# Kernel tuning notes

Hardware: AMD Instinct MI355X
Metric: run time of the kernel (lower is better)

The kernel has to match this reference:

```python
import jax, jax.numpy as jnp
import numpy as np

BLOCK = 32      # config.BLOCK_SIZE
PSF_WN = 64     # config.PSF_WINDOW_N (upsampled block size == PSF kernel size)
DX = 1e-06      # config.PIX_SIZE


def images_to_blocks(imgs, B):
    # Faithful to torch reshape/permute chain: block order is (nBW outer, nBH inner)
    N, H, W = imgs.shape
    nBH, nBW = H // B, W // B
    x = imgs.reshape(N, nBH, B, nBW, B)
    x = jnp.transpose(x, (0, 2, 4, 3, 1))        # [N,B,B,nBW,nBH]
    x = x.reshape(N, B, B, nBW * nBH)
    return jnp.transpose(x, (0, 3, 1, 2))        # [N,P,B,B]


def upsample_nearest(blocks, U):
    # torch F.interpolate(mode='nearest'): src index = floor(dst * B / U)
    N, P, B, _ = blocks.shape
    idx = (jnp.arange(U) * B) // U
    return blocks[:, :, idx[:, None], idx[None, :]]  # [N,P,U,U]


def depthwise_full_conv(x, w):
    # per-region cross-correlation with padding K-1 ("full"), groups=P
    N, P, K, _ = x.shape
    return jax.lax.conv_general_dilated(
        x, w[:, None, :, :], window_strides=(1, 1),
        padding=[(K - 1, K - 1), (K - 1, K - 1)],
        dimension_numbers=('NCHW', 'OIHW', 'NCHW'),
        feature_group_count=P)                   # [N,P,2K-1,2K-1]


def splat_blocks_to_sensor(block_out, x_centers, y_centers, X_N, Y_N, dx):
    # Vectorized scatter-add replacing the per-region python loop; out-of-bounds dropped
    N, P, Hk, Wk = block_out.shape
    hk = Hk // 2
    cx, cy = X_N // 2, Y_N // 2
    ic = cx + jnp.round(x_centers / dx).astype(jnp.int32)   # [P]
    jc = cy + jnp.round(y_centers / dx).astype(jnp.int32)
    I = ic[:, None] - hk + jnp.arange(Hk)                   # [P,Hk]
    J = jc[:, None] - hk + jnp.arange(Wk)                   # [P,Wk]
    lin = I[:, :, None] * Y_N + J[:, None, :]               # [P,Hk,Wk]
    ok = ((I >= 0) & (I < X_N))[:, :, None] & ((J >= 0) & (J < Y_N))[:, None, :]
    lin = jnp.where(ok, lin, -1).reshape(-1)
    sensor = jnp.zeros((N, X_N * Y_N), block_out.dtype)
    sensor = sensor.at[:, lin].add(block_out.reshape(N, -1), mode='drop')
    return sensor.reshape(N, X_N, Y_N)


def setup_inputs() -> dict:
    key = jax.random.key(0)
    k1, k2 = jax.random.split(key)
    N, H, W = 8, 512, 512
    P = (H // BLOCK) * (W // BLOCK)   # 256
    X_N = Y_N = 1024
    imgs = jax.random.uniform(k1, (N, H, W), jnp.float32)
    psf_stack = jax.random.uniform(k2, (P, PSF_WN, PSF_WN), jnp.float32)
    psf_stack = psf_stack / jnp.sum(psf_stack, axis=(1, 2), keepdims=True)
    # 16x16 grid of physical region centers, 48-pixel pitch (integer pixels so round() is exact)
    grid = jnp.arange(P)
    rows = (grid % 16).astype(jnp.float32)
    cols = (grid // 16).astype(jnp.float32)
    x_centers = (rows - 7.0) * 48.0 * DX
    y_centers = (cols - 7.0) * 48.0 * DX
    Xg, Yg = jnp.meshgrid(jnp.arange(X_N, dtype=jnp.float32) * DX,
                          jnp.arange(Y_N, dtype=jnp.float32) * DX, indexing='ij')
    return {"imgs": imgs, "psf_stack": psf_stack, "X": Xg, "Y": Yg,
            "x_centers": x_centers, "y_centers": y_centers}


def reference(imgs, psf_stack, X, Y, x_centers, y_centers):
    blocks = images_to_blocks(imgs, BLOCK)               # [N,P,32,32]
    blocks_up = upsample_nearest(blocks, PSF_WN)         # [N,P,64,64]
    block_out = depthwise_full_conv(blocks_up, psf_stack)  # [N,P,127,127]
    X_N, Y_N = X.shape
    return splat_blocks_to_sensor(block_out, x_centers, y_centers, X_N, Y_N, DX)
```

## Files before the change

kernel.cpp:

```cpp
#include <hip/hip_runtime.h>

typedef _Float16 h8 __attribute__((ext_vector_type(8)));
typedef float    f4 __attribute__((ext_vector_type(4)));
typedef unsigned int u4 __attribute__((ext_vector_type(4)));

#define IMG_N 8
#define IMG_H 512
#define IMG_W 512
#define P_CNT 256
#define PSFN  64
#define SENS  1024

#define TILE_HALVES 16384
#define TILES_BYTES ((size_t)IMG_N * P_CNT * TILE_HALVES * 2)

#define KW     90
#define KWB    (KW * 16)
#define KFRAG_PER_P (4 * 33 * KW)

#define BT_COLS   97
#define BT_HALVES (BT_COLS * 40)

__global__ __launch_bounds__(256) void svconv_prep(
    const float* __restrict__ psf, u4* __restrict__ kfrag)
{
    __shared__ float ps[PSFN * PSFN];
    __shared__ float Kc[4 * 33 * 33];
    const int p = blockIdx.x >> 2, q4 = blockIdx.x & 3, tid = threadIdx.x;

    const float4* pp = (const float4*)(psf + (size_t)p * PSFN * PSFN);
    float4* pd = (float4*)ps;
    for (int i = tid; i < PSFN * PSFN / 4; i += 256) pd[i] = pp[i];
    __syncthreads();

    for (int idx = tid; idx < 4 * 33 * 33; idx += 256) {
        const int g = idx % 33, e = (idx / 33) % 33, cls = idx / 1089;
        const int pi = cls >> 1, pj = cls & 1;
        const int E = pi ? 32 : 33;
        float sv = 0.f;
        if (e < E) {
            const int a = 2 * e - 1 + pi, b = 2 * g - 1 + pj;
            #pragma unroll
            for (int du = 0; du < 2; ++du) {
                const int x = a + du;
                if ((unsigned)x < 64u) {
                    #pragma unroll
                    for (int dv = 0; dv < 2; ++dv) {
                        const int y = b + dv;
                        if ((unsigned)y < 64u) sv += ps[x * 64 + y];
                    }
                }
            }
        }
        Kc[idx] = sv;
    }
    __syncthreads();

    u4* kout = kfrag + (size_t)p * KFRAG_PER_P;
    for (int i2 = tid; i2 < KFRAG_PER_P / 4; i2 += 256) {
        const int idx = q4 * (KFRAG_PER_P / 4) + i2;
        const int w = idx % KW;
        const int g = (idx / KW) % 33;
        const int cls = idx / (KW * 33);
        h8 hv;
        #pragma unroll
        for (int j = 0; j < 8; ++j) {
            const int e = w + j - 32;
            const float v = ((unsigned)e < 33u) ? Kc[cls * 1089 + e * 33 + g] : 0.f;
            hv[j] = (_Float16)v;
        }
        kout[idx] = __builtin_bit_cast(u4, hv);
    }
}

__global__ __launch_bounds__(256, 4) void svconv_main(
    const float* __restrict__ imgs, const u4* __restrict__ kfrag,
    _Float16* __restrict__ tiles)
{
    __shared__ __align__(16) _Float16 BT[BT_HALVES];

    const int bid = blockIdx.x;
    const int n = bid >> 8, p = bid & 255;
    const int bh = p & 15, bw = p >> 4;
    const int tid = threadIdx.x;
    const int wv = tid >> 6, lane = tid & 63;
    const int m = lane & 15, q = lane >> 4;

    for (int i = tid; i < BT_HALVES; i += 256) BT[i] = (_Float16)0.f;
    __syncthreads();
    {
        const int r0 = tid >> 5, c = tid & 31;
        const float* src = imgs + ((size_t)n * IMG_H + bh * 32) * IMG_W + bw * 32;
        for (int r = r0; r < 32; r += 8)
            BT[(c + 32) * 40 + r] = (_Float16)src[r * IMG_W + c];
    }
    __syncthreads();

    const int cls = wv, pi = cls >> 1, pj = cls & 1;
    const int U0 = pi ? 31 : 32;
    const char* btc = (const char*)BT + pj * 80;

    int boff[4];
    #pragma unroll
    for (int vt = 0; vt < 4; ++vt) boff[vt] = (16 * vt + m) * 80 + q * 16;

    const char* ka[4];
    {
        const char* base = (const char*)(kfrag + (size_t)p * KFRAG_PER_P
                                         + cls * 33 * KW);
        #pragma unroll
        for (int ut = 0; ut < 4; ++ut) {
            const int t0 = 8 * q - m + (U0 - 16 * ut) + 32;
            ka[ut] = base + t0 * 16;
        }
    }

    f4 acc[4][4];
    #pragma unroll
    for (int ut = 0; ut < 4; ++ut)
        #pragma unroll
        for (int vt = 0; vt < 4; ++vt) acc[ut][vt] = (f4){0.f, 0.f, 0.f, 0.f};

    #pragma unroll 3
    for (int g = 0; g < 33; ++g) {
        h8 A[4];
        #pragma unroll
        for (int ut = 0; ut < 4; ++ut)
            A[ut] = __builtin_bit_cast(h8, *(const u4*)(ka[ut] + g * KWB));
        h8 B[4];
        #pragma unroll
        for (int vt = 0; vt < 4; ++vt)
            B[vt] = *(const h8*)(btc + boff[vt] + g * 80);
        #pragma unroll
        for (int ut = 0; ut < 4; ++ut)
            #pragma unroll
            for (int vt = 0; vt < 4; ++vt)
                acc[ut][vt] = __builtin_amdgcn_mfma_f32_16x16x32_f16(
                    A[ut], B[vt], acc[ut][vt], 0, 0, 0);
    }

    _Float16* tile = tiles + (size_t)(n * P_CNT + p) * TILE_HALVES;
    #pragma unroll
    for (int ut = 0; ut < 4; ++ut) {
        #pragma unroll
        for (int reg = 0; reg < 4; ++reg) {
            const int u = 16 * ut + 4 * q + reg;
            _Float16* rp = tile + (2 * u + pi) * 128 + 2 * m + pj;
            #pragma unroll
            for (int vt = 0; vt < 4; ++vt)
                rp[32 * vt] = (_Float16)acc[ut][vt][reg];
        }
    }
}

#define LSTRIDE 136
#define ZOFF    (48 * LSTRIDE)

__global__ __launch_bounds__(256) void svconv_gather(
    const _Float16* __restrict__ tiles, float* __restrict__ out)
{
    __shared__ __align__(16) _Float16 Ls[ZOFF + 8];

    const int bid = blockIdx.x;
    const int n = bid & 7, x = bid >> 3;
    const int tid = threadIdx.x;

    int bhlo = (x + 288) / 48 - 10; if (bhlo < 0) bhlo = 0;
    const int bhhi = (x < 113) ? -1 : (((x - 113) / 48) > 15 ? 15 : (x - 113) / 48);
    const _Float16* tn = tiles + (size_t)n * P_CNT * TILE_HALVES;

    for (int i = tid; i < (ZOFF + 8) / 8; i += 256)
        ((u4*)Ls)[i] = (u4){0u, 0u, 0u, 0u};
    __syncthreads();

    for (int c = tid; c < 768; c += 256) {
        const int w = c & 15, rid = c >> 4;
        const int k3 = rid >> 4, bww = rid & 15;
        const int bhh = bhlo + k3;
        if (bhh <= bhhi) {
            const int ti = x - 113 - 48 * bhh;
            const u4 val = *(const u4*)(tn + (size_t)(bww * 16 + bhh) * TILE_HALVES
                                        + ti * 128 + 8 * w);
            *(u4*)&Ls[rid * LSTRIDE + 8 * w] = val;
        }
    }
    __syncthreads();

    float* outrow = out + ((size_t)n << 20) + (size_t)x * SENS;
    if (tid == 0) outrow[0] = 0.f;
    #pragma unroll
    for (int hf = 0; hf < 2; ++hf) {
        const int k = tid + 256 * hf;
        const int y0 = 2 * k + 1, y1 = y0 + 1;
        int bwlo0 = (y0 + 288) / 48 - 10; if (bwlo0 < 0) bwlo0 = 0;
        const int bwhi0 = (y0 < 113) ? -1
                          : (((y0 - 113) / 48) > 15 ? 15 : (y0 - 113) / 48);
        int bwlo1 = (y1 + 288) / 48 - 10; if (bwlo1 < 0) bwlo1 = 0;
        const int bwhi1 = (y1 < 113 || y1 > 1023) ? -1
                          : (((y1 - 113) / 48) > 15 ? 15 : (y1 - 113) / 48);
        float s0 = 0.f, s1 = 0.f;
        #pragma unroll
        for (int kw = 0; kw < 4; ++kw) {
            const int bww = bwlo0 + kw;
            const bool ok0 = (bww <= bwhi0);
            const bool ok1 = (bww >= bwlo1) && (bww <= bwhi1);
            const int tj0 = y0 - 113 - 48 * bww;
            const int colbase = bww * LSTRIDE + tj0;
            #pragma unroll
            for (int k3 = 0; k3 < 3; ++k3) {
                const int idx = (ok0 | ok1) ? (k3 * 16 * LSTRIDE + colbase) : ZOFF;
                const unsigned v = *(const unsigned*)&Ls[idx];
                const float f0 = (float)__builtin_bit_cast(
                    _Float16, (unsigned short)(v & 0xffffu));
                const float f1 = (float)__builtin_bit_cast(
                    _Float16, (unsigned short)(v >> 16));
                s0 += ok0 ? f0 : 0.f;
                s1 += ok1 ? f1 : 0.f;
            }
        }
        outrow[y0] = s0;
        if (y1 <= 1023) outrow[y1] = s1;
    }
}

extern "C" void kernel_launch(void* const* d_in, const int* in_sizes, int n_in,
                              void* d_out, int out_size, void* d_ws, size_t ws_size,
                              hipStream_t stream) {
    const float* imgs = (const float*)d_in[0];
    const float* psf  = (const float*)d_in[1];
    float* out = (float*)d_out;
    _Float16* tiles = (_Float16*)d_ws;
    u4* kfrag = (u4*)((char*)d_ws + TILES_BYTES);

    svconv_prep<<<dim3(P_CNT * 4), dim3(256), 0, stream>>>(psf, kfrag);
    svconv_main<<<dim3(IMG_N * P_CNT), dim3(256), 0, stream>>>(imgs, kfrag, tiles);
    svconv_gather<<<dim3(IMG_N * SENS), dim3(256), 0, stream>>>(tiles, out);
}
```

Baseline: 206.7 us.

## Write conv tiles in sensor-row-major layout so gather reads contiguous rows

```diff
diff --git a/kernel.cpp b/kernel.cpp
--- a/kernel.cpp
+++ b/kernel.cpp
@@ -11,8 +11,9 @@
 #define PSFN  64
 #define SENS  1024
 
-#define TILE_HALVES 16384
-#define TILES_BYTES ((size_t)IMG_N * P_CNT * TILE_HALVES * 2)
+#define XROWS 847
+#define G_HALVES ((size_t)IMG_N * XROWS * 3 * 2048)
+#define G_BYTES  (G_HALVES * 2)
 
 #define KW     90
 #define KWB    (KW * 16)
@@ -75,7 +76,7 @@
 
 __global__ __launch_bounds__(256, 4) void svconv_main(
     const float* __restrict__ imgs, const u4* __restrict__ kfrag,
-    _Float16* __restrict__ tiles)
+    _Float16* __restrict__ G)
 {
     __shared__ __align__(16) _Float16 BT[BT_HALVES];
 
@@ -139,25 +140,30 @@
                     A[ut], B[vt], acc[ut][vt], 0, 0, 0);
     }
 
-    _Float16* tile = tiles + (size_t)(n * P_CNT + p) * TILE_HALVES;
+    _Float16* Gn = G + (size_t)n * XROWS * 3 * 2048;
     #pragma unroll
     for (int ut = 0; ut < 4; ++ut) {
         #pragma unroll
         for (int reg = 0; reg < 4; ++reg) {
             const int u = 16 * ut + 4 * q + reg;
-            _Float16* rp = tile + (2 * u + pi) * 128 + 2 * m + pj;
-            #pragma unroll
-            for (int vt = 0; vt < 4; ++vt)
-                rp[32 * vt] = (_Float16)acc[ut][vt][reg];
-        }
-    }
-}
-
-#define LSTRIDE 136
-#define ZOFF    (48 * LSTRIDE)
+            const int i = 2 * u + pi;
+            if (i < 127) {
+                const int d = (i + 17) / 48;
+                const int k = (bh < 2 - d) ? bh : (2 - d);
+                _Float16* rp = Gn + ((size_t)(48 * bh + i) * 3 + k) * 2048
+                               + bw * 128 + 2 * m + pj;
+                #pragma unroll
+                for (int vt = 0; vt < 4; ++vt)
+                    rp[32 * vt] = (_Float16)acc[ut][vt][reg];
+            }
+        }
+    }
+}
+
+#define ZOFF (3 * 2048)
 
 __global__ __launch_bounds__(256) void svconv_gather(
-    const _Float16* __restrict__ tiles, float* __restrict__ out)
+    const _Float16* __restrict__ G, float* __restrict__ out)
 {
     __shared__ __align__(16) _Float16 Ls[ZOFF + 8];
 
@@ -167,22 +173,17 @@
 
     int bhlo = (x + 288) / 48 - 10; if (bhlo < 0) bhlo = 0;
     const int bhhi = (x < 113) ? -1 : (((x - 113) / 48) > 15 ? 15 : (x - 113) / 48);
-    const _Float16* tn = tiles + (size_t)n * P_CNT * TILE_HALVES;
-
-    for (int i = tid; i < (ZOFF + 8) / 8; i += 256)
-        ((u4*)Ls)[i] = (u4){0u, 0u, 0u, 0u};
-    __syncthreads();
-
-    for (int c = tid; c < 768; c += 256) {
-        const int w = c & 15, rid = c >> 4;
-        const int k3 = rid >> 4, bww = rid & 15;
-        const int bhh = bhlo + k3;
-        if (bhh <= bhhi) {
-            const int ti = x - 113 - 48 * bhh;
-            const u4 val = *(const u4*)(tn + (size_t)(bww * 16 + bhh) * TILE_HALVES
-                                        + ti * 128 + 8 * w);
-            *(u4*)&Ls[rid * LSTRIDE + 8 * w] = val;
-        }
+    const int nvalid = bhhi - bhlo + 1;
+    const int xp = x - 113;
+
+    if (tid == 0) *(u4*)&Ls[ZOFF] = (u4){0u, 0u, 0u, 0u};
+    const u4* Gb = (const u4*)(G + ((size_t)n * XROWS + xp) * 3 * 2048);
+    #pragma unroll
+    for (int k3 = 0; k3 < 3; ++k3) {
+        u4 val = (u4){0u, 0u, 0u, 0u};
+        if ((unsigned)xp < (unsigned)XROWS && k3 < nvalid)
+            val = Gb[k3 * 256 + tid];
+        *(u4*)&Ls[(k3 * 256 + tid) * 8] = val;
     }
     __syncthreads();
 
@@ -205,10 +206,10 @@
             const bool ok0 = (bww <= bwhi0);
             const bool ok1 = (bww >= bwlo1) && (bww <= bwhi1);
             const int tj0 = y0 - 113 - 48 * bww;
-            const int colbase = bww * LSTRIDE + tj0;
+            const int colbase = bww * 128 + tj0;
             #pragma unroll
             for (int k3 = 0; k3 < 3; ++k3) {
-                const int idx = (ok0 | ok1) ? (k3 * 16 * LSTRIDE + colbase) : ZOFF;
+                const int idx = (ok0 | ok1) ? (k3 * 2048 + colbase) : ZOFF;
                 const unsigned v = *(const unsigned*)&Ls[idx];
                 const float f0 = (float)__builtin_bit_cast(
                     _Float16, (unsigned short)(v & 0xffffu));
@@ -229,10 +230,10 @@
     const float* imgs = (const float*)d_in[0];
     const float* psf  = (const float*)d_in[1];
     float* out = (float*)d_out;
-    _Float16* tiles = (_Float16*)d_ws;
-    u4* kfrag = (u4*)((char*)d_ws + TILES_BYTES);
+    _Float16* G = (_Float16*)d_ws;
+    u4* kfrag = (u4*)((char*)d_ws + G_BYTES);
 
     svconv_prep<<<dim3(P_CNT * 4), dim3(256), 0, stream>>>(psf, kfrag);
-    svconv_main<<<dim3(IMG_N * P_CNT), dim3(256), 0, stream>>>(imgs, kfrag, tiles);
-    svconv_gather<<<dim3(IMG_N * SENS), dim3(256), 0, stream>>>(tiles, out);
-}
+    svconv_main<<<dim3(IMG_N * P_CNT), dim3(256), 0, stream>>>(imgs, kfrag, G);
+    svconv_gather<<<dim3(IMG_N * SENS), dim3(256), 0, stream>>>(G, out);
+}
```

After: 205.2 us. Within noise of the previous version (-0.7%).
